# Kernel tuning notes

Hardware: AMD Instinct MI355X
Metric: run time of the kernel (lower is better)

Reference implementation:

```python
import jax, jax.numpy as jnp
import numpy as np

HEADS = 16
DIM_HEAD = 64
SCALE = DIM_HEAD ** -0.5


def setup_inputs() -> dict:
    key = jax.random.key(0)
    k1, k2, k3 = jax.random.split(key, 3)
    B, N, D = 4, 4096, 1024
    inner = HEADS * DIM_HEAD  # 1024
    x = jax.random.normal(k1, (B, N, D), dtype=jnp.float32)
    w_qkv = jax.random.normal(k2, (D, 3 * inner), dtype=jnp.float32) * (D ** -0.5)
    w_out = jax.random.normal(k3, (inner, D), dtype=jnp.float32) * (inner ** -0.5)
    b_out = jnp.zeros((D,), dtype=jnp.float32)
    return {"x": x, "w_qkv": w_qkv, "w_out": w_out, "b_out": b_out}


def reference(x, w_qkv, w_out, b_out):
    B, N, D = x.shape
    inner = HEADS * DIM_HEAD
    qkv = x @ w_qkv  # [B, N, 3*inner]
    q, k, v = jnp.split(qkv, 3, axis=-1)

    def to_heads(t):  # [B, N, inner] -> [B, H, N, Dh]
        return t.reshape(B, N, HEADS, DIM_HEAD).transpose(0, 2, 1, 3)

    q, k, v = to_heads(q), to_heads(k), to_heads(v)
    q = jax.nn.softmax(q * SCALE, axis=-1)   # softmax over feature dim d
    k = jax.nn.softmax(k, axis=-2)           # softmax over sequence dim n
    # context[d, e] = sum_n q[n, d] * k[n, e]
    context = jnp.einsum('bhnd,bhne->bhde', q, k)
    # out[n, e] = sum_d context[d, e] * v[n, d]
    out = jnp.einsum('bhde,bhnd->bhne', context, v)
    out = out.transpose(0, 2, 1, 3).reshape(B, N, inner)  # [B, N, inner]
    return out @ w_out + b_out
```

## Files before the change

### kernel.cpp

```cpp
#include <hip/hip_runtime.h>
#include <hip/hip_bf16.h>

#define SEQ    4096
#define SCALE  0.125f

typedef __attribute__((ext_vector_type(8))) short s8v;
typedef __attribute__((ext_vector_type(4))) float f4v;

__device__ __forceinline__ unsigned short f2bf(float f){
  unsigned int u = __builtin_bit_cast(unsigned int, f);
  u += 0x7FFFu + ((u >> 16) & 1u);
  return (unsigned short)(u >> 16);
}
__device__ __forceinline__ float bf2f(unsigned short s){
  unsigned int u = ((unsigned int)s) << 16;
  return __builtin_bit_cast(float, u);
}

typedef const __attribute__((address_space(1))) unsigned int gl_uint;
typedef __attribute__((address_space(3))) unsigned int lds_uint;

__device__ __forceinline__ void gload_lds16(const unsigned short* g, unsigned short* l){
  __builtin_amdgcn_global_load_lds((gl_uint*)g, (lds_uint*)l, 16, 0, 0);
}

__global__ __launch_bounds__(256) void qkv_gemm(
    const unsigned short* __restrict__ A,
    const unsigned short* __restrict__ Bt,
    unsigned short* __restrict__ qt,
    unsigned short* __restrict__ kt,
    unsigned short* __restrict__ vb)
{
  __shared__ unsigned short sA[128*32];
  __shared__ unsigned short sB[128*32];
  const int K = 1024;
  const int tid  = threadIdx.x;
  const int wave = tid >> 6, lane = tid & 63;
  const int quad = lane >> 4, l16 = lane & 15;
  const int bid = blockIdx.x;
  const int per = 16 * 24;
  const int st = bid / per, rr = bid % per;
  const int bm = (st * 16 + (rr % 16)) * 128;
  const int bn = (rr / 16) * 128;
  const int wm = (wave >> 1) * 64, wn = (wave & 1) * 64;

  f4v acc[4][4];
#pragma unroll
  for (int i = 0; i < 4; i++)
#pragma unroll
    for (int j = 0; j < 4; j++) acc[i][j] = (f4v){0.f,0.f,0.f,0.f};

  const unsigned short* ap = A  + (size_t)(bm + (tid >> 2)) * K + (tid & 3) * 8;
  const unsigned short* bp = Bt + (size_t)(bn + (tid >> 2)) * K + (tid & 3) * 8;
  unsigned short* sAw = sA + wave * 512;
  unsigned short* sBw = sB + wave * 512;

  for (int k0 = 0; k0 < K; k0 += 32){
    __syncthreads();
    gload_lds16(ap + k0,                    sAw);
    gload_lds16(ap + (size_t)64 * K + k0,   sAw + 2048);
    gload_lds16(bp + k0,                    sBw);
    gload_lds16(bp + (size_t)64 * K + k0,   sBw + 2048);
    __syncthreads();
    s8v af[4], bf[4];
#pragma unroll
    for (int mt = 0; mt < 4; mt++) af[mt] = *(const s8v*)&sA[(wm + mt*16 + l16)*32 + quad*8];
#pragma unroll
    for (int nt = 0; nt < 4; nt++) bf[nt] = *(const s8v*)&sB[(wn + nt*16 + l16)*32 + quad*8];
#pragma unroll
    for (int mt = 0; mt < 4; mt++)
#pragma unroll
      for (int nt = 0; nt < 4; nt++)
        acc[mt][nt] = __builtin_amdgcn_mfma_f32_16x16x32_bf16(af[mt], bf[nt], acc[mt][nt], 0, 0, 0);
  }

  const int colbase = bn + wn;
  const int sec = colbase >> 10;

  if (sec == 2){
#pragma unroll
    for (int nt = 0; nt < 4; nt++){
      int vc = colbase + nt*16 + l16 - 2048;
#pragma unroll
      for (int mt = 0; mt < 4; mt++){
        int row = bm + wm + mt*16 + quad*4;
#pragma unroll
        for (int r = 0; r < 4; r++)
          vb[(size_t)(row + r) * 1024 + vc] = f2bf(acc[mt][nt][r]);
      }
    }
    return;
  }

  if (sec == 0){
#pragma unroll
    for (int mt = 0; mt < 4; mt++){
#pragma unroll
      for (int r = 0; r < 4; r++){
        float m = fmaxf(fmaxf(acc[mt][0][r], acc[mt][1][r]),
                        fmaxf(acc[mt][2][r], acc[mt][3][r]));
        for (int off = 8; off; off >>= 1) m = fmaxf(m, __shfl_xor(m, off));
        m *= SCALE;
        float e0 = __expf(acc[mt][0][r] * SCALE - m);
        float e1 = __expf(acc[mt][1][r] * SCALE - m);
        float e2 = __expf(acc[mt][2][r] * SCALE - m);
        float e3 = __expf(acc[mt][3][r] * SCALE - m);
        float s = (e0 + e1) + (e2 + e3);
        for (int off = 8; off; off >>= 1) s += __shfl_xor(s, off);
        float inv = 1.f / s;
        acc[mt][0][r] = e0 * inv; acc[mt][1][r] = e1 * inv;
        acc[mt][2][r] = e2 * inv; acc[mt][3][r] = e3 * inv;
      }
    }
  }

  unsigned short* dst = sec ? kt : qt;
#pragma unroll
  for (int nt = 0; nt < 4; nt++){
    int col = colbase + nt*16 + l16;
    int h = (col >> 6) & 15;
    int de = col & 63;
#pragma unroll
    for (int mt = 0; mt < 4; mt++){
      int row = bm + wm + mt*16 + quad*4;
      int bb = row >> 12;
      int nl = row & 4095;
      ushort4 o;
      o.x = f2bf(acc[mt][nt][0]); o.y = f2bf(acc[mt][nt][1]);
      o.z = f2bf(acc[mt][nt][2]); o.w = f2bf(acc[mt][nt][3]);
      *(ushort4*)&dst[(((size_t)bb * 16 + h) * 64 + de) * SEQ + nl] = o;
    }
  }
}

__global__ __launch_bounds__(256) void gemm_final(
    const unsigned short* __restrict__ A,
    const unsigned short* __restrict__ C2t,
    float* __restrict__ Cf,
    const float* __restrict__ bias)
{
  __shared__ unsigned short sA[128*32];
  __shared__ unsigned short sB[128*32];
  const int K = 1024;
  const int tid  = threadIdx.x;
  const int wave = tid >> 6, lane = tid & 63;
  const int quad = lane >> 4, l16 = lane & 15;
  const int bid = blockIdx.x;
  const int per = 16 * 8;
  const int st = bid / per, rr = bid % per;
  const int by = st * 16 + (rr % 16);
  const int bm = by * 128;
  const int bn = (rr / 16) * 128;
  const int b  = by >> 5;
  const unsigned short* Bt = C2t + (size_t)b * 1024 * 1024;
  const int wm = (wave >> 1) * 64, wn = (wave & 1) * 64;

  f4v acc[4][4];
#pragma unroll
  for (int i = 0; i < 4; i++)
#pragma unroll
    for (int j = 0; j < 4; j++) acc[i][j] = (f4v){0.f,0.f,0.f,0.f};

  const unsigned short* ap = A  + (size_t)(bm + (tid >> 2)) * K + (tid & 3) * 8;
  const unsigned short* bp = Bt + (size_t)(bn + (tid >> 2)) * K + (tid & 3) * 8;
  unsigned short* sAw = sA + wave * 512;
  unsigned short* sBw = sB + wave * 512;

  for (int k0 = 0; k0 < K; k0 += 32){
    __syncthreads();
    gload_lds16(ap + k0,                    sAw);
    gload_lds16(ap + (size_t)64 * K + k0,   sAw + 2048);
    gload_lds16(bp + k0,                    sBw);
    gload_lds16(bp + (size_t)64 * K + k0,   sBw + 2048);
    __syncthreads();
    s8v af[4], bf[4];
#pragma unroll
    for (int mt = 0; mt < 4; mt++) af[mt] = *(const s8v*)&sA[(wm + mt*16 + l16)*32 + quad*8];
#pragma unroll
    for (int nt = 0; nt < 4; nt++) bf[nt] = *(const s8v*)&sB[(wn + nt*16 + l16)*32 + quad*8];
#pragma unroll
    for (int mt = 0; mt < 4; mt++)
#pragma unroll
      for (int nt = 0; nt < 4; nt++)
        acc[mt][nt] = __builtin_amdgcn_mfma_f32_16x16x32_bf16(af[mt], bf[nt], acc[mt][nt], 0, 0, 0);
  }

#pragma unroll
  for (int nt = 0; nt < 4; nt++){
    int col = bn + wn + nt*16 + l16;
    float bv = bias[col];
#pragma unroll
    for (int mt = 0; mt < 4; mt++){
      int row = bm + wm + mt*16 + quad*4;
#pragma unroll
      for (int r = 0; r < 4; r++)
        Cf[(size_t)(row + r) * 1024 + col] = acc[mt][nt][r] + bv;
    }
  }
}

__global__ void cvt_f32_bf16(const float4* __restrict__ in, ushort4* __restrict__ outp){
  int i = blockIdx.x * 256 + threadIdx.x;
  float4 v = in[i];
  ushort4 o;
  o.x = f2bf(v.x); o.y = f2bf(v.y); o.z = f2bf(v.z); o.w = f2bf(v.w);
  outp[i] = o;
}

__global__ __launch_bounds__(256) void transpose_cvt(const float* __restrict__ in,
                                                     unsigned short* __restrict__ outp,
                                                     int R, int C){
  __shared__ float tile[64][65];
  int r0 = blockIdx.y * 64, c0 = blockIdx.x * 64;
  int t = threadIdx.x;
  for (int i = t; i < 4096; i += 256){ int r = i >> 6, c = i & 63;
    tile[r][c] = in[(size_t)(r0 + r) * C + c0 + c]; }
  __syncthreads();
  for (int i = t; i < 4096; i += 256){ int c = i >> 6, r = i & 63;
    outp[(size_t)(c0 + c) * R + r0 + r] = f2bf(tile[r][c]); }
}

__global__ __launch_bounds__(256) void sm_k(unsigned short* __restrict__ kt){
  __shared__ float sred[8];
  int row = blockIdx.x;
  int t = threadIdx.x, wave = t >> 6, lane = t & 63;
  unsigned short* base = kt + (size_t)row * SEQ + t * 16;
  float v[16];
#pragma unroll
  for (int i = 0; i < 16; i++) v[i] = bf2f(base[i]);
  float m = -1e30f;
#pragma unroll
  for (int i = 0; i < 16; i++) m = fmaxf(m, v[i]);
  for (int o = 32; o; o >>= 1) m = fmaxf(m, __shfl_down(m, o));
  if (!lane) sred[wave] = m;
  __syncthreads();
  m = fmaxf(fmaxf(sred[0], sred[1]), fmaxf(sred[2], sred[3]));
  float s = 0.f;
#pragma unroll
  for (int i = 0; i < 16; i++){ v[i] = __expf(v[i] - m); s += v[i]; }
  for (int o = 32; o; o >>= 1) s += __shfl_down(s, o);
  if (!lane) sred[4 + wave] = s;
  __syncthreads();
  s = (sred[4] + sred[5]) + (sred[6] + sred[7]);
  float inv = 1.f / s;
#pragma unroll
  for (int i = 0; i < 16; i++) base[i] = f2bf(v[i] * inv);
}

__global__ __launch_bounds__(256) void ctx_partial(const unsigned short* __restrict__ qt,
                                                   const unsigned short* __restrict__ kt,
                                                   float* __restrict__ ctxp){
  __shared__ float red[4096];
  int bh = blockIdx.x >> 2, ch = blockIdx.x & 3;
  int t = threadIdx.x, wave = t >> 6, lane = t & 63, quad = lane >> 4, l16 = lane & 15;
  const unsigned short* qb = qt + (size_t)bh * 64 * SEQ;
  const unsigned short* kb = kt + (size_t)bh * 64 * SEQ;
  f4v acc[4][4];
#pragma unroll
  for (int i = 0; i < 4; i++)
#pragma unroll
    for (int j = 0; j < 4; j++) acc[i][j] = (f4v){0.f,0.f,0.f,0.f};
  int ns = ch * 1024 + wave * 256;
  for (int n0 = ns; n0 < ns + 256; n0 += 32){
    s8v af[4], bf[4];
#pragma unroll
    for (int mt = 0; mt < 4; mt++) af[mt] = *(const s8v*)&qb[(size_t)(mt*16 + l16) * SEQ + n0 + quad*8];
#pragma unroll
    for (int nt = 0; nt < 4; nt++) bf[nt] = *(const s8v*)&kb[(size_t)(nt*16 + l16) * SEQ + n0 + quad*8];
#pragma unroll
    for (int mt = 0; mt < 4; mt++)
#pragma unroll
      for (int nt = 0; nt < 4; nt++)
        acc[mt][nt] = __builtin_amdgcn_mfma_f32_16x16x32_bf16(af[mt], bf[nt], acc[mt][nt], 0, 0, 0);
  }
  for (int i = t; i < 4096; i += 256) red[i] = 0.f;
  __syncthreads();
  for (int w = 0; w < 4; w++){
    if (wave == w){
#pragma unroll
      for (int mt = 0; mt < 4; mt++)
#pragma unroll
        for (int nt = 0; nt < 4; nt++)
#pragma unroll
          for (int r = 0; r < 4; r++)
            red[(mt*16 + quad*4 + r) * 64 + nt*16 + l16] += acc[mt][nt][r];
    }
    __syncthreads();
  }
  float* cp = ctxp + (size_t)blockIdx.x * 4096;
  for (int i = t; i < 4096; i += 256) cp[i] = red[i];
}

__global__ __launch_bounds__(256) void ctx2_kernel(const float* __restrict__ ctxp,
                                                   const float* __restrict__ w_out,
                                                   unsigned short* __restrict__ ctx2t){
  __shared__ float ctxs[4096];
  int bh = blockIdx.x >> 4, fc = blockIdx.x & 15;
  int b = bh >> 4, h = bh & 15;
  int t = threadIdx.x;
  int fl = t & 63, dg = t >> 6;
  int f = fc * 64 + fl;
  for (int i = t; i < 4096; i += 256){
    const float* p = ctxp + (size_t)bh * 4 * 4096 + i;
    ctxs[i] = (p[0] + p[4096]) + (p[8192] + p[12288]);
  }
  __syncthreads();
  float acc[16];
#pragma unroll
  for (int i = 0; i < 16; i++) acc[i] = 0.f;
  for (int e = 0; e < 64; e++){
    float w = w_out[(size_t)(h * 64 + e) * 1024 + f];
#pragma unroll
    for (int dd = 0; dd < 16; dd++)
      acc[dd] += ctxs[(dg * 16 + dd) * 64 + e] * w;
  }
  unsigned short* op = ctx2t + ((size_t)b * 1024 + f) * 1024 + h * 64 + dg * 16;
#pragma unroll
  for (int g = 0; g < 4; g++){
    ushort4 o;
    o.x = f2bf(acc[g*4+0]); o.y = f2bf(acc[g*4+1]);
    o.z = f2bf(acc[g*4+2]); o.w = f2bf(acc[g*4+3]);
    *(ushort4*)&op[g*4] = o;
  }
}

extern "C" void kernel_launch(void* const* d_in, const int* in_sizes, int n_in,
                              void* d_out, int out_size, void* d_ws, size_t ws_size,
                              hipStream_t stream) {
  const float* x     = (const float*)d_in[0];
  const float* w_qkv = (const float*)d_in[1];
  const float* w_out = (const float*)d_in[2];
  const float* b_out = (const float*)d_in[3];
  float* out = (float*)d_out;

  const int M = 4 * SEQ;

  unsigned short* xb = (unsigned short*)d_out;

  char* wp = (char*)d_ws;
  size_t off = 0;
  auto nxt = [&](size_t bytes) -> char* {
    char* p = wp + off;
    off += (bytes + 255) & ~(size_t)255;
    return p;
  };
  unsigned short* wqkvT = (unsigned short*)nxt((size_t)3072 * 1024 * 2);
  unsigned short* qt    = (unsigned short*)nxt((size_t)64 * 64 * SEQ * 2);
  unsigned short* kt    = (unsigned short*)nxt((size_t)64 * 64 * SEQ * 2);
  unsigned short* vb    = (unsigned short*)nxt((size_t)M * 1024 * 2);
  float*          ctxp  = (float*)wqkvT;
  unsigned short* ctx2t = qt;

  cvt_f32_bf16<<<(M * 1024) / 4 / 256, 256, 0, stream>>>((const float4*)x, (ushort4*)xb);
  transpose_cvt<<<dim3(3072 / 64, 1024 / 64), 256, 0, stream>>>(w_qkv, wqkvT, 1024, 3072);

  qkv_gemm<<<(3072 / 128) * (M / 128), 256, 0, stream>>>(xb, wqkvT, qt, kt, vb);

  sm_k<<<64 * 64, 256, 0, stream>>>(kt);

  ctx_partial<<<64 * 4, 256, 0, stream>>>(qt, kt, ctxp);

  ctx2_kernel<<<64 * 16, 256, 0, stream>>>(ctxp, w_out, ctx2t);

  gemm_final<<<(1024 / 128) * (M / 128), 256, 0, stream>>>(vb, ctx2t, out, b_out);
}
```

Before: 395.9 us.

## Fuse K softmax into QKV GEMM epilogue with deferred normalization via atomics

Removes the separate sm_k pass over K. The QKV GEMM epilogue now computes exp(k) directly, reduces per-column partial sums and atomically accumulates them into a ksum buffer. The 1/sum normalization is folded into the context reduction in ctx2_kernel. Because no max is subtracted, exp can overflow for large K values, and the float atomics make the summation order nondeterministic. The GEMM block ordering is also changed from a grouped swizzle to a plain 2D grid, which may reduce L2 reuse.

```diff
diff --git a/kernel.cpp b/kernel.cpp
--- a/kernel.cpp
+++ b/kernel.cpp
@@ -29,7 +29,8 @@
     const unsigned short* __restrict__ Bt,
     unsigned short* __restrict__ qt,
     unsigned short* __restrict__ kt,
-    unsigned short* __restrict__ vb)
+    unsigned short* __restrict__ vb,
+    float* __restrict__ ksum)
 {
   __shared__ unsigned short sA[128*32];
   __shared__ unsigned short sB[128*32];
@@ -37,11 +38,7 @@
   const int tid  = threadIdx.x;
   const int wave = tid >> 6, lane = tid & 63;
   const int quad = lane >> 4, l16 = lane & 15;
-  const int bid = blockIdx.x;
-  const int per = 16 * 24;
-  const int st = bid / per, rr = bid % per;
-  const int bm = (st * 16 + (rr % 16)) * 128;
-  const int bn = (rr / 16) * 128;
+  const int bm = blockIdx.y * 128, bn = blockIdx.x * 128;
   const int wm = (wave >> 1) * 64, wn = (wave & 1) * 64;
 
   f4v acc[4][4];
@@ -92,6 +89,7 @@
     return;
   }
 
+  float psum[4];
   if (sec == 0){
 #pragma unroll
     for (int mt = 0; mt < 4; mt++){
@@ -112,6 +110,22 @@
         acc[mt][2][r] = e2 * inv; acc[mt][3][r] = e3 * inv;
       }
     }
+  } else {
+#pragma unroll
+    for (int nt = 0; nt < 4; nt++){
+      float s = 0.f;
+#pragma unroll
+      for (int mt = 0; mt < 4; mt++)
+#pragma unroll
+        for (int r = 0; r < 4; r++){
+          float e = __expf(acc[mt][nt][r]);
+          acc[mt][nt][r] = e;
+          s += e;
+        }
+      s += __shfl_xor(s, 16);
+      s += __shfl_xor(s, 32);
+      psum[nt] = s;
+    }
   }
 
   unsigned short* dst = sec ? kt : qt;
@@ -131,6 +145,21 @@
       *(ushort4*)&dst[(((size_t)bb * 16 + h) * 64 + de) * SEQ + nl] = o;
     }
   }
+
+  if (sec == 1 && quad == 0){
+    int bb = bm >> 12;
+#pragma unroll
+    for (int nt = 0; nt < 4; nt++){
+      int col = colbase + nt*16 + l16;
+      int h = (col >> 6) & 15;
+      int e = col & 63;
+      atomicAdd(&ksum[((bb * 16 + h) << 6) + e], psum[nt]);
+    }
+  }
+}
+
+__global__ void zero_ksum(float* __restrict__ ksum){
+  ksum[blockIdx.x * 256 + threadIdx.x] = 0.f;
 }
 
 __global__ __launch_bounds__(256) void gemm_final(
@@ -145,13 +174,8 @@
   const int tid  = threadIdx.x;
   const int wave = tid >> 6, lane = tid & 63;
   const int quad = lane >> 4, l16 = lane & 15;
-  const int bid = blockIdx.x;
-  const int per = 16 * 8;
-  const int st = bid / per, rr = bid % per;
-  const int by = st * 16 + (rr % 16);
-  const int bm = by * 128;
-  const int bn = (rr / 16) * 128;
-  const int b  = by >> 5;
+  const int bm = blockIdx.y * 128, bn = blockIdx.x * 128;
+  const int b  = blockIdx.y >> 5;
   const unsigned short* Bt = C2t + (size_t)b * 1024 * 1024;
   const int wm = (wave >> 1) * 64, wn = (wave & 1) * 64;
 
@@ -220,33 +244,6 @@
     outp[(size_t)(c0 + c) * R + r0 + r] = f2bf(tile[r][c]); }
 }
 
-__global__ __launch_bounds__(256) void sm_k(unsigned short* __restrict__ kt){
-  __shared__ float sred[8];
-  int row = blockIdx.x;
-  int t = threadIdx.x, wave = t >> 6, lane = t & 63;
-  unsigned short* base = kt + (size_t)row * SEQ + t * 16;
-  float v[16];
-#pragma unroll
-  for (int i = 0; i < 16; i++) v[i] = bf2f(base[i]);
-  float m = -1e30f;
-#pragma unroll
-  for (int i = 0; i < 16; i++) m = fmaxf(m, v[i]);
-  for (int o = 32; o; o >>= 1) m = fmaxf(m, __shfl_down(m, o));
-  if (!lane) sred[wave] = m;
-  __syncthreads();
-  m = fmaxf(fmaxf(sred[0], sred[1]), fmaxf(sred[2], sred[3]));
-  float s = 0.f;
-#pragma unroll
-  for (int i = 0; i < 16; i++){ v[i] = __expf(v[i] - m); s += v[i]; }
-  for (int o = 32; o; o >>= 1) s += __shfl_down(s, o);
-  if (!lane) sred[4 + wave] = s;
-  __syncthreads();
-  s = (sred[4] + sred[5]) + (sred[6] + sred[7]);
-  float inv = 1.f / s;
-#pragma unroll
-  for (int i = 0; i < 16; i++) base[i] = f2bf(v[i] * inv);
-}
-
 __global__ __launch_bounds__(256) void ctx_partial(const unsigned short* __restrict__ qt,
                                                    const unsigned short* __restrict__ kt,
                                                    float* __restrict__ ctxp){
@@ -293,6 +290,7 @@
 
 __global__ __launch_bounds__(256) void ctx2_kernel(const float* __restrict__ ctxp,
                                                    const float* __restrict__ w_out,
+                                                   const float* __restrict__ ksum,
                                                    unsigned short* __restrict__ ctx2t){
   __shared__ float ctxs[4096];
   int bh = blockIdx.x >> 4, fc = blockIdx.x & 15;
@@ -302,7 +300,8 @@
   int f = fc * 64 + fl;
   for (int i = t; i < 4096; i += 256){
     const float* p = ctxp + (size_t)bh * 4 * 4096 + i;
-    ctxs[i] = (p[0] + p[4096]) + (p[8192] + p[12288]);
+    float inv = 1.f / ksum[(bh << 6) + (i & 63)];
+    ctxs[i] = ((p[0] + p[4096]) + (p[8192] + p[12288])) * inv;
   }
   __syncthreads();
   float acc[16];
@@ -348,19 +347,19 @@
   unsigned short* qt    = (unsigned short*)nxt((size_t)64 * 64 * SEQ * 2);
   unsigned short* kt    = (unsigned short*)nxt((size_t)64 * 64 * SEQ * 2);
   unsigned short* vb    = (unsigned short*)nxt((size_t)M * 1024 * 2);
+  float*          ksum  = (float*)nxt((size_t)64 * 64 * 4);
   float*          ctxp  = (float*)wqkvT;
   unsigned short* ctx2t = qt;
 
+  zero_ksum<<<16, 256, 0, stream>>>(ksum);
   cvt_f32_bf16<<<(M * 1024) / 4 / 256, 256, 0, stream>>>((const float4*)x, (ushort4*)xb);
   transpose_cvt<<<dim3(3072 / 64, 1024 / 64), 256, 0, stream>>>(w_qkv, wqkvT, 1024, 3072);
 
-  qkv_gemm<<<(3072 / 128) * (M / 128), 256, 0, stream>>>(xb, wqkvT, qt, kt, vb);
-
-  sm_k<<<64 * 64, 256, 0, stream>>>(kt);
+  qkv_gemm<<<dim3(3072 / 128, M / 128), 256, 0, stream>>>(xb, wqkvT, qt, kt, vb, ksum);
 
   ctx_partial<<<64 * 4, 256, 0, stream>>>(qt, kt, ctxp);
 
-  ctx2_kernel<<<64 * 16, 256, 0, stream>>>(ctxp, w_out, ctx2t);
-
-  gemm_final<<<(1024 / 128) * (M / 128), 256, 0, stream>>>(vb, ctx2t, out, b_out);
-}
+  ctx2_kernel<<<64 * 16, 256, 0, stream>>>(ctxp, w_out, ksum, ctx2t);
+
+  gemm_final<<<dim3(1024 / 128, M / 128), 256, 0, stream>>>(vb, ctx2t, out, b_out);
+}
```

Result: slower. 489.1 us (+23.5%).
